# Optimization experiments

Measured on AMD Instinct MI355X. Metric: run time of the kernel, lower is better.

The kernel has to match this reference:

```python
import jax, jax.numpy as jnp
import numpy as np

TOTAL_TOKENS = 2_000_000
N_READS = 2000
DIM_HIDDEN = 128
VOCAB = 4


def setup_inputs() -> dict:
    key = jax.random.key(0)
    k1, k2, k3 = jax.random.split(key, 3)
    tokens = jax.random.randint(k1, (TOTAL_TOKENS,), 0, VOCAB, dtype=jnp.int64 if jax.config.jax_enable_x64 else jnp.int32)
    segment_ids = jnp.sort(jax.random.randint(k2, (TOTAL_TOKENS,), 0, N_READS, dtype=jnp.int32))
    embedding = jax.random.normal(k3, (VOCAB, DIM_HIDDEN), dtype=jnp.float32)
    return {"tokens": tokens, "segment_ids": segment_ids, "embedding": embedding, "n_reads": N_READS}


def reference(tokens, segment_ids, embedding, n_reads):
    # Per-read: gather base embeddings then mean over the read -> segment-mean.
    gathered = embedding[tokens]                                   # [T, D]
    sums = jax.ops.segment_sum(gathered, segment_ids, num_segments=n_reads)   # [R, D]
    counts = jax.ops.segment_sum(jnp.ones_like(tokens, dtype=embedding.dtype),
                                 segment_ids, num_segments=n_reads)           # [R]
    counts = jnp.maximum(counts, 1.0)  # guard empty segments (torch loop never has empty reads)
    return sums / counts[:, None]
```

## Files before the change

kernel.cpp:

```cpp
#include <hip/hip_runtime.h>
#include <stdint.h>


#define TPB 256
#define TOK_PER_THREAD 32
#define DIM 128
#define VOCAB 4

__global__ __launch_bounds__(TPB) void seq_count_kernel(
    const int* __restrict__ tokens,
    const int* __restrict__ segs,
    unsigned long long* __restrict__ counts,
    int T) {
  const long long base =
      ((long long)blockIdx.x * TPB + threadIdx.x) * TOK_PER_THREAD;
  if (base >= T) return;

  int cur_seg = -1;
  unsigned long long acc = 0ULL;

#pragma unroll
  for (int g = 0; g < TOK_PER_THREAD / 4; ++g) {
    const long long i = base + (long long)g * 4;
    if (i + 4 <= (long long)T) {
      const int4 tk = *(const int4*)(tokens + i);
      const int4 sg = *(const int4*)(segs + i);
      const int tks[4] = {tk.x, tk.y, tk.z, tk.w};
      const int sgs[4] = {sg.x, sg.y, sg.z, sg.w};
#pragma unroll
      for (int j = 0; j < 4; ++j) {
        const int s = sgs[j];
        if (s != cur_seg) {
          if (acc) atomicAdd(&counts[cur_seg], acc);
          cur_seg = s;
          acc = 0ULL;
        }
        acc += 1ULL << (16 * (tks[j] & 3));
      }
    } else {
      for (long long k = i; k < (long long)T && k < i + 4; ++k) {
        const int s = segs[k];
        if (s != cur_seg) {
          if (acc) atomicAdd(&counts[cur_seg], acc);
          cur_seg = s;
          acc = 0ULL;
        }
        acc += 1ULL << (16 * (tokens[k] & 3));
      }
    }
  }
  if (acc && cur_seg >= 0) atomicAdd(&counts[cur_seg], acc);
}

__global__ __launch_bounds__(DIM) void seq_emit_kernel(
    const unsigned long long* __restrict__ counts,
    const float* __restrict__ emb,
    float* __restrict__ out) {
  const int seg = blockIdx.x;
  const int d = threadIdx.x;
  const unsigned long long c = counts[seg];
  const float c0 = (float)(unsigned)(c & 0xFFFFULL);
  const float c1 = (float)(unsigned)((c >> 16) & 0xFFFFULL);
  const float c2 = (float)(unsigned)((c >> 32) & 0xFFFFULL);
  const float c3 = (float)(unsigned)((c >> 48) & 0xFFFFULL);
  const float tot = fmaxf(c0 + c1 + c2 + c3, 1.0f);
  const float v = c0 * emb[0 * DIM + d] + c1 * emb[1 * DIM + d] +
                  c2 * emb[2 * DIM + d] + c3 * emb[3 * DIM + d];
  out[(long long)seg * DIM + d] = v / tot;
}

extern "C" void kernel_launch(void* const* d_in, const int* in_sizes, int n_in,
                              void* d_out, int out_size, void* d_ws,
                              size_t ws_size, hipStream_t stream) {
  const int* tokens = (const int*)d_in[0];
  const int* segs = (const int*)d_in[1];
  const float* emb = (const float*)d_in[2];
  float* out = (float*)d_out;

  const int T = in_sizes[0];
  const int n_reads = out_size / DIM;

  unsigned long long* counts = (unsigned long long*)d_ws;

  hipMemsetAsync(counts, 0, (size_t)n_reads * sizeof(unsigned long long),
                 stream);

  const int tok_per_block = TPB * TOK_PER_THREAD;
  const int nblk = (int)(((long long)T + tok_per_block - 1) / tok_per_block);
  seq_count_kernel<<<nblk, TPB, 0, stream>>>(tokens, segs, counts, T);
  seq_emit_kernel<<<n_reads, DIM, 0, stream>>>(counts, emb, out);
}
```

Measured before the change: 82.12 us.

## Fuse count and emit into one per-segment kernel using wave binary search

Replaces the memset, atomic counting kernel and emit kernel with a single kernel that launches one block per segment. Each block finds its segment's bounds in the sorted segment_ids using a 64-way wave-parallel binary search, counts token types with packed 16-bit counters, reduces the counts across the block, and writes the mean. This removes the atomics, the memset and two extra launches, and the kernel no longer reads the segment array except for search probes. In exchange, each block does a dependent chain of global-memory search probes, token loads are not vectorized, and only about 1000 tokens per segment are spread over 256 threads.

```diff
diff --git a/kernel.cpp b/kernel.cpp
--- a/kernel.cpp
+++ b/kernel.cpp
@@ -2,71 +2,75 @@
 #include <stdint.h>
 
 
+#define DIM 128
 #define TPB 256
-#define TOK_PER_THREAD 32
-#define DIM 128
-#define VOCAB 4
 
-__global__ __launch_bounds__(TPB) void seq_count_kernel(
-    const int* __restrict__ tokens,
-    const int* __restrict__ segs,
-    unsigned long long* __restrict__ counts,
-    int T) {
-  const long long base =
-      ((long long)blockIdx.x * TPB + threadIdx.x) * TOK_PER_THREAD;
-  if (base >= T) return;
+__device__ __forceinline__ int wave_lower_bound(const int* __restrict__ a,
+                                                int n, int t) {
+  const int lane = threadIdx.x & 63;
+  int lo = 0, hi = n;
+  while (hi - lo > 64) {
+    const long long span = hi - lo;
+    const int idx = lo + (int)((span * (lane + 1)) >> 6);
+    const int probe = (idx < hi) ? a[idx] : 0x7fffffff;
+    const unsigned long long mask = __ballot(probe >= t);
+    const int first = __ffsll(mask) - 1;
+    const int nlo = (first == 0) ? lo : lo + (int)((span * (long long)first) >> 6);
+    const int nhi = lo + (int)((span * (long long)(first + 1)) >> 6);
+    lo = nlo;
+    hi = nhi;
+  }
+  const int idx = lo + lane;
+  const bool ge = (idx < hi) ? (a[idx] >= t) : true;
+  const unsigned long long mask = __ballot(ge);
+  return lo + __ffsll(mask) - 1;
+}
 
-  int cur_seg = -1;
+__global__ __launch_bounds__(TPB) void seg_mean_kernel(
+    const int* __restrict__ tokens, const int* __restrict__ segs,
+    const float* __restrict__ emb, float* __restrict__ out, int T) {
+  const int s = blockIdx.x;
+  const int tid = threadIdx.x;
+  const int wave = tid >> 6;
+
+  __shared__ int bounds[2];
+  __shared__ unsigned long long red[TPB / 64];
+
+  if (wave < 2) {
+    const int r = wave_lower_bound(segs, T, s + wave);
+    if ((tid & 63) == 0) bounds[wave] = r;
+  }
+  __syncthreads();
+  const int lo = bounds[0];
+  const int hi = bounds[1];
+
   unsigned long long acc = 0ULL;
+  for (int i = lo + tid; i < hi; i += TPB) {
+    acc += 1ULL << ((tokens[i] & 3) << 4);
+  }
 
 #pragma unroll
-  for (int g = 0; g < TOK_PER_THREAD / 4; ++g) {
-    const long long i = base + (long long)g * 4;
-    if (i + 4 <= (long long)T) {
-      const int4 tk = *(const int4*)(tokens + i);
-      const int4 sg = *(const int4*)(segs + i);
-      const int tks[4] = {tk.x, tk.y, tk.z, tk.w};
-      const int sgs[4] = {sg.x, sg.y, sg.z, sg.w};
-#pragma unroll
-      for (int j = 0; j < 4; ++j) {
-        const int s = sgs[j];
-        if (s != cur_seg) {
-          if (acc) atomicAdd(&counts[cur_seg], acc);
-          cur_seg = s;
-          acc = 0ULL;
-        }
-        acc += 1ULL << (16 * (tks[j] & 3));
-      }
-    } else {
-      for (long long k = i; k < (long long)T && k < i + 4; ++k) {
-        const int s = segs[k];
-        if (s != cur_seg) {
-          if (acc) atomicAdd(&counts[cur_seg], acc);
-          cur_seg = s;
-          acc = 0ULL;
-        }
-        acc += 1ULL << (16 * (tokens[k] & 3));
-      }
-    }
+  for (int off = 32; off > 0; off >>= 1) {
+    acc += __shfl_down(acc, off, 64);
   }
-  if (acc && cur_seg >= 0) atomicAdd(&counts[cur_seg], acc);
-}
+  if ((tid & 63) == 0) red[wave] = acc;
+  __syncthreads();
+  if (tid == 0) {
+    red[0] = red[0] + red[1] + red[2] + red[3];
+  }
+  __syncthreads();
 
-__global__ __launch_bounds__(DIM) void seq_emit_kernel(
-    const unsigned long long* __restrict__ counts,
-    const float* __restrict__ emb,
-    float* __restrict__ out) {
-  const int seg = blockIdx.x;
-  const int d = threadIdx.x;
-  const unsigned long long c = counts[seg];
-  const float c0 = (float)(unsigned)(c & 0xFFFFULL);
-  const float c1 = (float)(unsigned)((c >> 16) & 0xFFFFULL);
-  const float c2 = (float)(unsigned)((c >> 32) & 0xFFFFULL);
-  const float c3 = (float)(unsigned)((c >> 48) & 0xFFFFULL);
-  const float tot = fmaxf(c0 + c1 + c2 + c3, 1.0f);
-  const float v = c0 * emb[0 * DIM + d] + c1 * emb[1 * DIM + d] +
-                  c2 * emb[2 * DIM + d] + c3 * emb[3 * DIM + d];
-  out[(long long)seg * DIM + d] = v / tot;
+  const unsigned long long c = red[0];
+  if (tid < DIM) {
+    const float c0 = (float)(unsigned)(c & 0xFFFFULL);
+    const float c1 = (float)(unsigned)((c >> 16) & 0xFFFFULL);
+    const float c2 = (float)(unsigned)((c >> 32) & 0xFFFFULL);
+    const float c3 = (float)(unsigned)((c >> 48) & 0xFFFFULL);
+    const float tot = fmaxf(c0 + c1 + c2 + c3, 1.0f);
+    const float v = c0 * emb[tid] + c1 * emb[DIM + tid] +
+                    c2 * emb[2 * DIM + tid] + c3 * emb[3 * DIM + tid];
+    out[(long long)s * DIM + tid] = v / tot;
+  }
 }
 
 extern "C" void kernel_launch(void* const* d_in, const int* in_sizes, int n_in,
@@ -80,13 +84,5 @@
   const int T = in_sizes[0];
   const int n_reads = out_size / DIM;
 
-  unsigned long long* counts = (unsigned long long*)d_ws;
-
-  hipMemsetAsync(counts, 0, (size_t)n_reads * sizeof(unsigned long long),
-                 stream);
-
-  const int tok_per_block = TPB * TOK_PER_THREAD;
-  const int nblk = (int)(((long long)T + tok_per_block - 1) / tok_per_block);
-  seq_count_kernel<<<nblk, TPB, 0, stream>>>(tokens, segs, counts, T);
-  seq_emit_kernel<<<n_reads, DIM, 0, stream>>>(counts, emb, out);
+  seg_mean_kernel<<<n_reads, TPB, 0, stream>>>(tokens, segs, emb, out, T);
 }
```

New measurement: 71.36 us, median of 2. 1.15x faster.
